# Kernel optimization log

Hardware: AMD Instinct MI355X
Metric: run time of the kernel (lower is better)

The kernel has to match this reference:

```python
import jax, jax.numpy as jnp
import numpy as np

B, S, N = 16, 64, 4096
D = 64            # input_dim*seq_len == output_dim*graph_dim
FEAT = 64
E = 32768
HEADS = (3, 3, 1)
NEG_SLOPE = 0.2   # PyG GATConv default negative_slope


def _lin_init(key, fi, fo):
    k1, k2 = jax.random.split(key)
    s = 1.0 / np.sqrt(fi)
    return (jax.random.uniform(k1, (fi, fo), jnp.float32, -s, s),
            jax.random.uniform(k2, (fo,), jnp.float32, -s, s))


def setup_inputs() -> dict:
    key = jax.random.key(0)
    ks = jax.random.split(key, 32)
    inp = {}
    inp["inputs"] = jax.random.normal(ks[0], (B, S, N, 1), jnp.float32)
    inp["edge_index"] = jax.random.randint(ks[1], (2, E), 0, N, dtype=jnp.int32)
    inp["W_seq"], inp["b_seq"] = _lin_init(ks[2], D, D)
    inp["src_embed"] = jax.random.normal(ks[3], (N, FEAT), jnp.float32) * 0.1
    inp["tgt_embed"] = jax.random.normal(ks[4], (FEAT, N), jnp.float32) * 0.1
    for i, H in enumerate(HEADS):
        s = 1.0 / np.sqrt(D)
        inp[f"Wg{i}"] = jax.random.uniform(ks[5 + 5 * i], (D, H * D), jnp.float32, -s, s)
        inp[f"asrc{i}"] = jax.random.normal(ks[6 + 5 * i], (H, D), jnp.float32) * 0.1
        inp[f"adst{i}"] = jax.random.normal(ks[7 + 5 * i], (H, D), jnp.float32) * 0.1
        inp[f"bg{i}"] = jnp.zeros((D,), jnp.float32)
        inp[f"Wl{i}"], inp[f"bl{i}"] = _lin_init(ks[8 + 5 * i], D, D)
    inp["Wo"], inp["bo"] = _lin_init(ks[25], D, D)
    return inp


def _gat(x, src, dst, W, a_src, a_dst, b):
    # PyG GATConv, concat=False (mean over heads). x: [B,N,D] -> [B,N,D]
    H, C = a_src.shape
    xp = jnp.einsum('bnd,dhc->bnhc', x, W.reshape(D, H, C))       # [B,N,H,C]
    al_s = jnp.einsum('bnhc,hc->bnh', xp, a_src)
    al_d = jnp.einsum('bnhc,hc->bnh', xp, a_dst)
    e = jax.nn.leaky_relu(al_s[:, src] + al_d[:, dst], NEG_SLOPE)  # [B,Et,H]

    def per_graph(e_b, xj_b):
        m = jax.ops.segment_max(e_b, dst, num_segments=N)          # [N,H]
        w = jnp.exp(e_b - m[dst])
        z = jax.ops.segment_sum(w, dst, num_segments=N)
        alpha = w / z[dst]                                         # softmax per dst node
        return jax.ops.segment_sum(xj_b * alpha[..., None], dst, num_segments=N)

    out = jax.vmap(per_graph)(e, xp[:, src])                       # [B,N,H,C]
    return out.mean(axis=2) + b


def _forward(inputs, edge_index, W_seq, b_seq, src_embed, tgt_embed,
             Wg0, asrc0, adst0, bg0, Wl0, bl0,
             Wg1, asrc1, adst1, bg1, Wl1, bl1,
             Wg2, asrc2, adst2, bg2, Wl2, bl2, Wo, bo):
    loop = jnp.arange(N, dtype=edge_index.dtype)
    src = jnp.concatenate([edge_index[0], loop])   # PyG add_self_loops=True
    dst = jnp.concatenate([edge_index[1], loop])
    h = inputs.transpose(0, 2, 3, 1).reshape(B * N, D)
    h = h @ W_seq + b_seq + h                       # seq_linear residual
    A = jax.nn.softmax(jax.nn.relu(src_embed @ tgt_embed), axis=1)  # learned adjacency [N,N]
    gat_p = [(Wg0, asrc0, adst0, bg0), (Wg1, asrc1, adst1, bg1), (Wg2, asrc2, adst2, bg2)]
    lin_p = [(Wl0, bl0), (Wl1, bl1), (Wl2, bl2)]
    for i in range(3):
        hb = h.reshape(B, N, D)
        # layer-0 GAT output is computed but unused in the original code (dead); skip it
        h_cur = _gat(hb, src, dst, *gat_p[i]).reshape(B * N, D) if i > 0 else None
        adp = jnp.einsum('mn,bnd->bmd', A, hb)      # adaptive-graph matmul (dropout in eval = identity)
        adp = (adp @ lin_p[i][0] + lin_p[i][1]).reshape(B * N, D)
        g = jax.nn.sigmoid(adp)
        if i == 0:
            origin = h @ Wo + bo
            h = jnp.tanh(h) * g + origin * (1.0 - g)
        elif i == 1:
            h = jax.nn.leaky_relu(h_cur, 0.01) * g + h * (1.0 - g)
        else:
            h = jax.nn.relu(h_cur) * g + h * (1.0 - g)
    return h.reshape(B, N, 1, D)   # [batch, node_num, output_dim, graph_dim]


def reference(inputs, edge_index, W_seq, b_seq, src_embed, tgt_embed,
              Wg0, asrc0, adst0, bg0, Wl0, bl0,
              Wg1, asrc1, adst1, bg1, Wl1, bl1,
              Wg2, asrc2, adst2, bg2, Wl2, bl2, Wo, bo):
    return _forward(inputs, edge_index, W_seq, b_seq, src_embed, tgt_embed,
                    Wg0, asrc0, adst0, bg0, Wl0, bl0,
                    Wg1, asrc1, adst1, bg1, Wl1, bl1,
                    Wg2, asrc2, adst2, bg2, Wl2, bl2, Wo, bo)
```

## Files before the change

kernel.cpp:

```cpp
#include <hip/hip_runtime.h>
#include <stdint.h>

#define NB 16
#define NN 4096
#define DD 64
#define EE 32768
#define ETOT 36864
#define ROWS 65536
#define KSPLIT 2

typedef _Float16 f16;
typedef f16   half8 __attribute__((ext_vector_type(8)));
typedef f16   f16x8 __attribute__((ext_vector_type(8)));
typedef f16   f16x4 __attribute__((ext_vector_type(4)));
typedef float f32x4 __attribute__((ext_vector_type(4)));

__device__ __forceinline__ void gload16(const f16* g, f16* l) {
  __builtin_amdgcn_global_load_lds((const __attribute__((address_space(1))) void*)g,
                                   (__attribute__((address_space(3))) void*)l, 16, 0, 0);
}

__global__ __launch_bounds__(256) void k_zero2(int* a, int* b) {
  int i = blockIdx.x * 256 + threadIdx.x;
  if (i < NN) a[i] = 0;
  else if (i < 2 * NN) b[i - NN] = 0;
}

__global__ __launch_bounds__(256) void k_count(const int* __restrict__ ei, int* __restrict__ cnt) {
  int t = blockIdx.x * 256 + threadIdx.x;
  if (t >= ETOT) return;
  int d = (t < EE) ? ei[EE + t] : (t - EE);
  atomicAdd(&cnt[d], 1);
}

__global__ __launch_bounds__(256) void k_scan(const int* __restrict__ cnt, int* __restrict__ offs) {
  __shared__ int part[256];
  int t = threadIdx.x;
  int loc[16]; int s = 0;
  #pragma unroll
  for (int i = 0; i < 16; ++i) { int v = cnt[(t << 4) + i]; loc[i] = s; s += v; }
  part[t] = s;
  __syncthreads();
  int own = s;
  for (int d = 1; d < 256; d <<= 1) {
    int u = (t >= d) ? part[t - d] : 0;
    __syncthreads();
    part[t] += u;
    __syncthreads();
  }
  int base = part[t] - own;
  #pragma unroll
  for (int i = 0; i < 16; ++i) offs[(t << 4) + i] = base + loc[i];
}

__global__ __launch_bounds__(256) void k_fill(const int* __restrict__ ei, const int* __restrict__ offs,
                                              int* __restrict__ cur, int* __restrict__ esrc,
                                              int* __restrict__ edst) {
  int t = blockIdx.x * 256 + threadIdx.x;
  if (t >= ETOT) return;
  int s, d;
  if (t < EE) { s = ei[t]; d = ei[EE + t]; } else { s = d = t - EE; }
  int p = atomicAdd(&cur[d], 1);
  esrc[offs[d] + p] = s;
  edst[offs[d] + p] = d;
}

__global__ __launch_bounds__(256) void k_seq(const float* __restrict__ inp, const float* __restrict__ Wseq,
                                             const float* __restrict__ bseq, float* __restrict__ h) {
  __shared__ float X[64 * 68];
  int t = threadIdx.x;
  int b = blockIdx.x >> 6, n0 = (blockIdx.x & 63) << 6;
  #pragma unroll
  for (int i = 0; i < 16; ++i) {
    int idx = t + (i << 8);
    int s = idx >> 6, nl = idx & 63;
    X[nl * 68 + s] = inp[((size_t)((b << 6) + s) << 12) + n0 + nl];
  }
  __syncthreads();
  int c = t & 63, rg = t >> 6;
  float Wc[64];
  #pragma unroll
  for (int k = 0; k < 64; ++k) Wc[k] = Wseq[(k << 6) + c];
  float bc = bseq[c];
  for (int rr = 0; rr < 16; ++rr) {
    int r = (rg << 4) + rr;
    float a = bc + X[r * 68 + c];
    #pragma unroll
    for (int k4 = 0; k4 < 16; ++k4) {
      float4 x = *(const float4*)&X[r * 68 + (k4 << 2)];
      a = fmaf(x.x, Wc[4*k4+0], a); a = fmaf(x.y, Wc[4*k4+1], a);
      a = fmaf(x.z, Wc[4*k4+2], a); a = fmaf(x.w, Wc[4*k4+3], a);
    }
    h[((size_t)(b << 12) + n0 + r) * 64 + c] = a;
  }
}

__global__ __launch_bounds__(256) void k_cast(const float* __restrict__ SE, const float* __restrict__ TE,
                                              f16* __restrict__ SEh, f16* __restrict__ TEh) {
  __shared__ float X[64 * 65];
  int t = threadIdx.x;
  if (blockIdx.x < 256) {
    int i = (blockIdx.x * 256 + t) * 4;
    float4 v = *(const float4*)(SE + i);
    f16 o[4] = {(f16)v.x, (f16)v.y, (f16)v.z, (f16)v.w};
    *(uint64_t*)(SEh + i) = *(uint64_t*)o;
    return;
  }
  int j0 = (blockIdx.x - 256) << 6;
  #pragma unroll
  for (int i = 0; i < 16; ++i) {
    int idx = t + (i << 8);
    int k = idx >> 6, jl = idx & 63;
    X[jl * 65 + k] = TE[((size_t)k << 12) + j0 + jl];
  }
  __syncthreads();
  int jl = t >> 2, kg = t & 3;
  f16 o[16];
  #pragma unroll
  for (int i = 0; i < 16; ++i) o[i] = (f16)X[jl * 65 + (kg << 4) + i];
  f16* dst = TEh + ((size_t)(j0 + jl) << 6) + (kg << 4);
  *(uint64_t*)(dst + 0) = *(uint64_t*)(o + 0);
  *(uint64_t*)(dst + 4) = *(uint64_t*)(o + 4);
  *(uint64_t*)(dst + 8) = *(uint64_t*)(o + 8);
  *(uint64_t*)(dst + 12) = *(uint64_t*)(o + 12);
}

__global__ __launch_bounds__(256) void k_adjmm(const f16* __restrict__ SEh, const f16* __restrict__ TEh,
                                               f16* __restrict__ A, float* __restrict__ Zpart) {
  __shared__ f16 Al[2][128 * 32];
  __shared__ f16 Bl[2][128 * 32];
  const int t = threadIdx.x, lane = t & 63, w = t >> 6;
  const int m0 = blockIdx.y << 7, j0 = blockIdx.x << 7;
  const int l15 = lane & 15, lhi = lane >> 4;
  const int wm = (w >> 1) << 6, wj = (w & 1) << 6;
  f32x4 acc[4][4] = {};
  const int c0 = (w << 6) + lane;
  const int row0 = c0 >> 2, ko0 = (c0 & 3) << 3;
  const int c1 = c0 + 256;
  const int row1 = c1 >> 2, ko1 = (c1 & 3) << 3;
  const f16* ga0 = SEh + (size_t)(m0 + row0) * 64 + ko0;
  const f16* ga1 = SEh + (size_t)(m0 + row1) * 64 + ko1;
  const f16* gb0 = TEh + (size_t)(j0 + row0) * 64 + ko0;
  const f16* gb1 = TEh + (size_t)(j0 + row1) * 64 + ko1;
  #pragma unroll
  for (int kt = 0; kt < 2; ++kt) {
    const int kof = kt << 5;
    gload16(ga0 + kof, Al[kt] + c0 * 8);
    gload16(ga1 + kof, Al[kt] + c1 * 8);
    gload16(gb0 + kof, Bl[kt] + c0 * 8);
    gload16(gb1 + kof, Bl[kt] + c1 * 8);
  }
  __syncthreads();
  #pragma unroll
  for (int kt = 0; kt < 2; ++kt) {
    half8 af[4], bf[4];
    #pragma unroll
    for (int i = 0; i < 4; ++i) {
      af[i] = *(const half8*)(Al[kt] + (wm + i * 16 + l15) * 32 + lhi * 8);
      bf[i] = *(const half8*)(Bl[kt] + (wj + i * 16 + l15) * 32 + lhi * 8);
    }
    #pragma unroll
    for (int mi = 0; mi < 4; ++mi)
      #pragma unroll
      for (int nj = 0; nj < 4; ++nj)
        acc[mi][nj] = __builtin_amdgcn_mfma_f32_16x16x32_f16(af[mi], bf[nj], acc[mi][nj], 0, 0, 0);
  }
  float rs[4][4];
  #pragma unroll
  for (int mi = 0; mi < 4; ++mi)
    #pragma unroll
    for (int r = 0; r < 4; ++r) rs[mi][r] = 0.f;
  #pragma unroll
  for (int mi = 0; mi < 4; ++mi)
    #pragma unroll
    for (int nj = 0; nj < 4; ++nj)
      #pragma unroll
      for (int r = 0; r < 4; ++r) {
        int row = m0 + wm + mi * 16 + lhi * 4 + r;
        int col = j0 + wj + nj * 16 + l15;
        float e = __expf(fmaxf(acc[mi][nj][r], 0.f));
        f16 eh = (f16)e;
        A[((size_t)row << 12) + col] = eh;
        rs[mi][r] += (float)eh;
      }
  #pragma unroll
  for (int mi = 0; mi < 4; ++mi)
    #pragma unroll
    for (int r = 0; r < 4; ++r) {
      float s = rs[mi][r];
      s += __shfl_xor(s, 1); s += __shfl_xor(s, 2);
      s += __shfl_xor(s, 4); s += __shfl_xor(s, 8);
      rs[mi][r] = s;
    }
  if (l15 == 0) {
    int p = (blockIdx.x << 1) + (w & 1);
    #pragma unroll
    for (int mi = 0; mi < 4; ++mi)
      #pragma unroll
      for (int r = 0; r < 4; ++r)
        Zpart[((size_t)p << 12) + m0 + wm + mi * 16 + lhi * 4 + r] = rs[mi][r];
  }
}

__global__ __launch_bounds__(256) void k_rowz(const float* __restrict__ Zpart, float* __restrict__ rowZ) {
  int row = blockIdx.x * 256 + threadIdx.x;
  float s = 0.f;
  #pragma unroll 8
  for (int p = 0; p < 64; ++p) s += Zpart[((size_t)p << 12) + row];
  rowZ[row] = 1.f / s;
}

#define NKT 32
__global__ __launch_bounds__(512) void k_gemm8(const f16* __restrict__ A, const f16* __restrict__ BT,
                                               f16* __restrict__ Cout) {
  extern __shared__ f16 smem[];
  const int t = threadIdx.x, lane = t & 63, wid = t >> 6;
  const int wr = wid >> 2, wc = wid & 3;
  const int l15 = lane & 15, lhi = lane >> 4;
  const int h7 = l15 & 7;
  const int wgid = blockIdx.x;
  const int nid = (wgid & 7) * 32 + (wgid >> 3);
  const int z = nid >> 7, rem = nid & 127;
  const int m0 = (rem >> 3) << 8;
  const int j0 = (rem & 7) << 7;
  const size_t kbase = (size_t)z << 11;
  f16* __restrict__ Cz = Cout + ((size_t)z << 22);

  const f16* gA[4]; int lA[4];
  #pragma unroll
  for (int i = 0; i < 4; ++i) {
    int s = t + (i << 9), row = s >> 3, sl = (s & 7) ^ (row & 7);
    gA[i] = A + (size_t)(m0 + row) * 4096 + kbase + sl * 8;
    lA[i] = s * 8;
  }
  const f16* gB[2]; int lB[2];
  #pragma unroll
  for (int i = 0; i < 2; ++i) {
    int s = t + (i << 9), row = s >> 3, sl = (s & 7) ^ (row & 7);
    gB[i] = BT + (size_t)(j0 + row) * 4096 + kbase + sl * 8;
    lB[i] = 16384 + s * 8;
  }
  #define SA(buf, kt, i) gload16(gA[i] + (kt) * 64, smem + (buf) * 24576 + lA[i])
  #define SB(buf, kt, i) gload16(gB[i] + (kt) * 64, smem + (buf) * 24576 + lB[i])

  const int rbase = wr << 7;
  const int cbase = wc << 5;
  f32x4 acc[8][2] = {};

  #pragma unroll
  for (int i = 0; i < 4; ++i) SA(0, 0, i);
  #pragma unroll
  for (int i = 0; i < 2; ++i) SB(0, 0, i);
  #pragma unroll
  for (int i = 0; i < 4; ++i) SA(1, 1, i);
  #pragma unroll
  for (int i = 0; i < 2; ++i) SB(1, 1, i);
  asm volatile("s_waitcnt vmcnt(6)" ::: "memory");
  __builtin_amdgcn_sched_barrier(0);
  __builtin_amdgcn_s_barrier();
  __builtin_amdgcn_sched_barrier(0);

  int b0 = 0, b1 = 1, b2 = 2;
  for (int kt = 0; kt < NKT; ++kt) {
    const f16* Ab = smem + b0 * 24576;
    const f16* Bb = Ab + 16384;
    const bool pf = (kt + 2 < NKT);
    {
      half8 af[8], bf[2];
      #pragma unroll
      for (int mi = 0; mi < 8; ++mi) {
        int row = rbase + mi * 16 + l15;
        af[mi] = *(const half8*)(Ab + row * 64 + (lhi ^ h7) * 8);
      }
      #pragma unroll
      for (int nj = 0; nj < 2; ++nj) {
        int row = cbase + nj * 16 + l15;
        bf[nj] = *(const half8*)(Bb + row * 64 + (lhi ^ h7) * 8);
      }
      if (pf) { SA(b2, kt + 2, 0); SA(b2, kt + 2, 1); SA(b2, kt + 2, 2); }
      __builtin_amdgcn_s_setprio(1);
      #pragma unroll
      for (int mi = 0; mi < 8; ++mi)
        #pragma unroll
        for (int nj = 0; nj < 2; ++nj)
          acc[mi][nj] = __builtin_amdgcn_mfma_f32_16x16x32_f16(af[mi], bf[nj], acc[mi][nj], 0, 0, 0);
      __builtin_amdgcn_s_setprio(0);
    }
    __builtin_amdgcn_s_barrier();
    __builtin_amdgcn_sched_barrier(0);
    {
      half8 af[8], bf[2];
      #pragma unroll
      for (int mi = 0; mi < 8; ++mi) {
        int row = rbase + mi * 16 + l15;
        af[mi] = *(const half8*)(Ab + row * 64 + ((4 + lhi) ^ h7) * 8);
      }
      #pragma unroll
      for (int nj = 0; nj < 2; ++nj) {
        int row = cbase + nj * 16 + l15;
        bf[nj] = *(const half8*)(Bb + row * 64 + ((4 + lhi) ^ h7) * 8);
      }
      if (pf) { SA(b2, kt + 2, 3); SB(b2, kt + 2, 0); SB(b2, kt + 2, 1); }
      __builtin_amdgcn_s_setprio(1);
      #pragma unroll
      for (int mi = 0; mi < 8; ++mi)
        #pragma unroll
        for (int nj = 0; nj < 2; ++nj)
          acc[mi][nj] = __builtin_amdgcn_mfma_f32_16x16x32_f16(af[mi], bf[nj], acc[mi][nj], 0, 0, 0);
      __builtin_amdgcn_s_setprio(0);
    }
    if (kt < NKT - 2)       asm volatile("s_waitcnt vmcnt(6)" ::: "memory");
    else if (kt == NKT - 2) asm volatile("s_waitcnt vmcnt(0)" ::: "memory");
    __builtin_amdgcn_sched_barrier(0);
    __builtin_amdgcn_s_barrier();
    __builtin_amdgcn_sched_barrier(0);
    int tb = b0; b0 = b1; b1 = b2; b2 = tb;
  }
  #undef SA
  #undef SB
  #pragma unroll
  for (int mi = 0; mi < 8; ++mi)
    #pragma unroll
    for (int nj = 0; nj < 2; ++nj)
      #pragma unroll
      for (int r = 0; r < 4; ++r) {
        int row = m0 + rbase + mi * 16 + (lhi << 2) + r;
        int col = j0 + cbase + nj * 16 + l15;
        Cz[(size_t)row * 1024 + col] = (f16)acc[mi][nj][r];
      }
}

template<int H, int NP>
__device__ __forceinline__ void wprep_body(const float* __restrict__ Wg, const float* __restrict__ asrc,
                                           const float* __restrict__ adst, const float* __restrict__ Wl,
                                           f16* __restrict__ Wgh, int bid, int t) {
  const int WL0 = H * 64 + 16;
  for (int i = bid * 256 + t; i < NP * 64; i += 16 * 256) {
    int j = i >> 6, k = i & 63;
    float v;
    if (j < H * 64) {
      v = Wg[(size_t)k * (H * 64) + j];
    } else if (j < H * 64 + 2 * H) {
      int cc = j - H * 64, hh = cc >> 1;
      const float* a = ((cc & 1) ? adst : asrc) + (hh << 6);
      const float* wrow = Wg + (size_t)k * (H * 64) + (hh << 6);
      float s = 0.f;
      #pragma unroll 16
      for (int c = 0; c < 64; ++c) s = fmaf(wrow[c], a[c], s);
      v = s;
    } else if (j >= WL0 && j < WL0 + 64) {
      v = Wl[(k << 6) + (j - WL0)];
    } else v = 0.f;
    Wgh[(size_t)j * 64 + k] = (f16)v;
  }
}

__global__ __launch_bounds__(256) void k_allprep(
    const float* __restrict__ Wg1, const float* __restrict__ as1, const float* __restrict__ ad1,
    const float* __restrict__ Wl1, f16* __restrict__ Wgh1,
    const float* __restrict__ Wg2, const float* __restrict__ as2, const float* __restrict__ ad2,
    const float* __restrict__ Wl2, f16* __restrict__ Wgh2,
    const float* __restrict__ Wl0, const float* __restrict__ Wo, f16* __restrict__ W0h) {
  int bid = blockIdx.x, t = threadIdx.x;
  if (bid < 16) wprep_body<3, 272>(Wg1, as1, ad1, Wl1, Wgh1, bid, t);
  else if (bid < 32) wprep_body<1, 144>(Wg2, as2, ad2, Wl2, Wgh2, bid - 16, t);
  else {
    for (int i = (bid - 32) * 256 + t; i < 128 * 64; i += 8 * 256) {
      int j = i >> 6, k = i & 63;
      float v = (j < 64) ? Wl0[(k << 6) + j] : Wo[(k << 6) + (j - 64)];
      W0h[(size_t)j * 64 + k] = (f16)v;
    }
  }
}

template<int H, int NP>
__global__ __launch_bounds__(256) void k_xpmm(const float* __restrict__ h, const f16* __restrict__ Wgh,
                                              f16* __restrict__ xp, float* __restrict__ als,
                                              float* __restrict__ ald, f16* __restrict__ HWlT) {
  const int WL0 = H * 64 + 16, JW0 = WL0 / 16, NT = NP / 16;
  __shared__ f16 Ah[64 * 72];
  __shared__ f16 Bh[NP * 72];
  __shared__ f16 stage[64 * 72];
  const int t = threadIdx.x, lane = t & 63, w = t >> 6;
  const size_t r0 = (size_t)blockIdx.x * 64;
  const int b = (int)(r0 >> 12), n0 = (int)(r0 & 4095);
  #pragma unroll
  for (int i = 0; i < 4; ++i) {
    int idx = t + (i << 8);
    int row = idx >> 4, k4 = (idx & 15) << 2;
    float4 v = *(const float4*)&h[(r0 + row) * 64 + k4];
    f16 o[4] = {(f16)v.x, (f16)v.y, (f16)v.z, (f16)v.w};
    *(uint64_t*)&Ah[row * 72 + k4] = *(uint64_t*)o;
  }
  for (int i = t; i < NP * 16; i += 256) {
    int row = i >> 4, k4 = (i & 15) << 2;
    *(uint64_t*)&Bh[row * 72 + k4] = *(const uint64_t*)&Wgh[(size_t)row * 64 + k4];
  }
  __syncthreads();
  const int l15 = lane & 15, lhi = lane >> 4;
  f32x4 acc[NT] = {};
  #pragma unroll
  for (int kk = 0; kk < 2; ++kk) {
    half8 af = *(const half8*)&Ah[(w * 16 + l15) * 72 + kk * 32 + lhi * 8];
    #pragma unroll
    for (int j = 0; j < NT; ++j) {
      half8 bf = *(const half8*)&Bh[(j * 16 + l15) * 72 + kk * 32 + lhi * 8];
      acc[j] = __builtin_amdgcn_mfma_f32_16x16x32_f16(af, bf, acc[j], 0, 0, 0);
    }
  }
  const int rl = w * 16 + lhi * 4;
  #pragma unroll
  for (int j = 0; j < NT; ++j) {
    int col = j * 16 + l15;
    if (j * 16 + 15 < H * 64) {
      #pragma unroll
      for (int r = 0; r < 4; ++r) {
        if (H == 3) xp[(r0 + rl + r) * 256 + ((col & 63) << 2) + (col >> 6)] = (f16)acc[j][r];
        else        xp[(r0 + rl + r) * 64 + col] = (f16)acc[j][r];
      }
    } else if (j < JW0) {
      int cc = col - H * 64;
      if (cc >= 0 && cc < 2 * H) {
        int hh = cc >> 1;
        #pragma unroll
        for (int r = 0; r < 4; ++r) {
          if (cc & 1) ald[(r0 + rl + r) * H + hh] = acc[j][r];
          else        als[(r0 + rl + r) * H + hh] = acc[j][r];
        }
      }
    } else {
      int e = col - WL0;
      f16 o[4] = {(f16)acc[j][0], (f16)acc[j][1], (f16)acc[j][2], (f16)acc[j][3]};
      *(uint64_t*)&stage[e * 72 + rl] = *(uint64_t*)o;
    }
  }
  __syncthreads();
  {
    int e = t >> 2, seg = (t & 3) << 4;
    float4 v0 = *(const float4*)&stage[e * 72 + seg];
    float4 v1 = *(const float4*)&stage[e * 72 + seg + 8];
    f16* dst = HWlT + (((size_t)((b << 6) + e)) << 12) + n0 + seg;
    *(float4*)dst = v0;
    *(float4*)(dst + 8) = v1;
  }
}

__global__ __launch_bounds__(256) void k_prep0(const float* __restrict__ h, const f16* __restrict__ W0h,
                                               f16* __restrict__ HWlT, f16* __restrict__ orig) {
  __shared__ f16 Ah[64 * 72];
  __shared__ f16 Bh[128 * 72];
  __shared__ f16 stage[64 * 72];
  const int t = threadIdx.x, lane = t & 63, w = t >> 6;
  const size_t r0 = (size_t)blockIdx.x * 64;
  const int b = (int)(r0 >> 12), n0 = (int)(r0 & 4095);
  #pragma unroll
  for (int i = 0; i < 4; ++i) {
    int idx = t + (i << 8);
    int row = idx >> 4, k4 = (idx & 15) << 2;
    float4 v = *(const float4*)&h[(r0 + row) * 64 + k4];
    f16 o[4] = {(f16)v.x, (f16)v.y, (f16)v.z, (f16)v.w};
    *(uint64_t*)&Ah[row * 72 + k4] = *(uint64_t*)o;
  }
  for (int i = t; i < 128 * 16; i += 256) {
    int row = i >> 4, k4 = (i & 15) << 2;
    *(uint64_t*)&Bh[row * 72 + k4] = *(const uint64_t*)&W0h[(size_t)row * 64 + k4];
  }
  __syncthreads();
  const int l15 = lane & 15, lhi = lane >> 4;
  f32x4 acc[8] = {};
  #pragma unroll
  for (int kk = 0; kk < 2; ++kk) {
    half8 af = *(const half8*)&Ah[(w * 16 + l15) * 72 + kk * 32 + lhi * 8];
    #pragma unroll
    for (int j = 0; j < 8; ++j) {
      half8 bf = *(const half8*)&Bh[(j * 16 + l15) * 72 + kk * 32 + lhi * 8];
      acc[j] = __builtin_amdgcn_mfma_f32_16x16x32_f16(af, bf, acc[j], 0, 0, 0);
    }
  }
  const int rl = w * 16 + lhi * 4;
  #pragma unroll
  for (int j = 0; j < 8; ++j) {
    int col = j * 16 + l15;
    if (j < 4) {
      f16 o[4] = {(f16)acc[j][0], (f16)acc[j][1], (f16)acc[j][2], (f16)acc[j][3]};
      *(uint64_t*)&stage[col * 72 + rl] = *(uint64_t*)o;
    } else {
      #pragma unroll
      for (int r = 0; r < 4; ++r)
        orig[(r0 + rl + r) * 64 + (col - 64)] = (f16)acc[j][r];
    }
  }
  __syncthreads();
  {
    int e = t >> 2, seg = (t & 3) << 4;
    float4 v0 = *(const float4*)&stage[e * 72 + seg];
    float4 v1 = *(const float4*)&stage[e * 72 + seg + 8];
    f16* dst = HWlT + (((size_t)((b << 6) + e)) << 12) + n0 + seg;
    *(float4*)dst = v0;
    *(float4*)(dst + 8) = v1;
  }
}

template<int H>
__global__ __launch_bounds__(256) void k_maxals(const float* __restrict__ als, float* __restrict__ Mals) {
  __shared__ float red[256];
  int b = blockIdx.x, t = threadIdx.x;
  size_t rbase = (size_t)b << 12;
  for (int h = 0; h < H; ++h) {
    float m = -1e30f;
    for (int n = t; n < NN; n += 256) m = fmaxf(m, als[(rbase + n) * H + h]);
    red[t] = m;
    __syncthreads();
    for (int d = 128; d; d >>= 1) {
      if (t < d) red[t] = fmaxf(red[t], red[t + d]);
      __syncthreads();
    }
    if (t == 0) Mals[b * H + h] = red[0];
    __syncthreads();
  }
}

template<int H>
__global__ __launch_bounds__(256) void k_wts(const float* __restrict__ als, const float* __restrict__ ald,
                                             const float* __restrict__ Mals, const int* __restrict__ esrc,
                                             const int* __restrict__ edst, float* __restrict__ wts) {
  const int WST = (H == 3) ? 4 : 1;
  int t = threadIdx.x, lane = t & 63, w = t >> 6;
  int gw = blockIdx.x * 4 + w;
  int b = gw & 15;
  int p = ((gw >> 4) << 6) + lane;
  size_t rbase = (size_t)b << 12;
  int s = esrc[p], n = edst[p];
  float* dst = wts + ((size_t)b * ETOT + p) * WST;
  #pragma unroll
  for (int h = 0; h < H; ++h) {
    float ad = ald[(rbase + n) * H + h];
    float B = Mals[b * H + h] + ad;
    float T = B > 0.f ? B : 0.2f * B;
    float ev = als[(rbase + s) * H + h] + ad;
    ev = ev > 0.f ? ev : 0.2f * ev;
    dst[h] = __expf(ev - T);
  }
}

template<int H>
__global__ __launch_bounds__(256) void k_agg(const f16* __restrict__ xp, const float* __restrict__ wts,
                                             const int* __restrict__ offs, const int* __restrict__ cnt,
                                             const int* __restrict__ esrc, const float* __restrict__ bg,
                                             float* __restrict__ hcur) {
  const int WST = (H == 3) ? 4 : 1;
  __shared__ float wbuf[4][64 * WST];
  __shared__ int   sbuf[4][64];
  int t = threadIdx.x, lane = t & 63, wv = t >> 6;
  int wid = (blockIdx.x << 2) + wv;
  int b = wid >> 12, n = wid & 4095;
  size_t rbase = (size_t)b << 12;
  int o = offs[n], c = cnt[n];
  const float* wsrc = wts + ((size_t)b * ETOT + o) * WST;
  float z[H], acc[H];
  #pragma unroll
  for (int hh = 0; hh < H; ++hh) { z[hh] = 0.f; acc[hh] = 0.f; }
  for (int e0 = 0; e0 < c; e0 += 64) {
    int ce = min(64, c - e0);
    if (lane < ce) {
      sbuf[wv][lane] = esrc[o + e0 + lane];
      if (H == 3) *(float4*)&wbuf[wv][lane * 4] = *(const float4*)&wsrc[(size_t)(e0 + lane) * 4];
      else        wbuf[wv][lane] = wsrc[e0 + lane];
    }
    #pragma unroll 4
    for (int e = 0; e < ce; ++e) {
      int s = sbuf[wv][e];
      if (H == 3) {
        float4 w4 = *(const float4*)&wbuf[wv][e * 4];
        f16x4 q = *(const f16x4*)(xp + (((size_t)(rbase + s)) << 8) + (lane << 2));
        z[0] += w4.x; acc[0] = fmaf(w4.x, (float)q[0], acc[0]);
        z[1] += w4.y; acc[1] = fmaf(w4.y, (float)q[1], acc[1]);
        z[2] += w4.z; acc[2] = fmaf(w4.z, (float)q[2], acc[2]);
      } else {
        float wv_ = wbuf[wv][e];
        float xv = (float)xp[(((size_t)(rbase + s)) << 6) + lane];
        z[0] += wv_; acc[0] = fmaf(wv_, xv, acc[0]);
      }
    }
  }
  float r = 0.f;
  #pragma unroll
  for (int hh = 0; hh < H; ++hh) r += acc[hh] / z[hh];
  hcur[(rbase + n) * 64 + lane] = r * (1.f / H) + bg[lane];
}

__global__ __launch_bounds__(256) void k_comb0e(const float* __restrict__ h, const f16* __restrict__ gp,
                                                const float* __restrict__ rowZ, const f16* __restrict__ orig,
                                                const float* __restrict__ bl, const float* __restrict__ bo,
                                                float* __restrict__ hout) {
  for (size_t i4 = (size_t)blockIdx.x * 256 + threadIdx.x; i4 < (size_t)ROWS * 16; i4 += (size_t)2048 * 256) {
    size_t i = i4 * 4;
    int d = (int)(i & 63), n = (int)((i >> 6) & 4095), b = (int)(i >> 18);
    size_t ga = ((size_t)n << 10) + (b << 6) + d;
    float zi = rowZ[n];
    f16x4 g0 = *(const f16x4*)&gp[ga];
    f16x4 g1 = *(const f16x4*)&gp[ga + (size_t)(4096 * 1024)];
    f16x4 og = *(const f16x4*)&orig[i];
    float4 hv = *(const float4*)&h[i];
    float4 o;
    float* op = &o.x;
    const float* hp = &hv.x;
    #pragma unroll
    for (int r = 0; r < 4; ++r) {
      float g = 1.f / (1.f + __expf(-(((float)g0[r] + (float)g1[r]) * zi + bl[d + r])));
      float orv = (float)og[r] + bo[d + r];
      op[r] = tanhf(hp[r]) * g + orv * (1.f - g);
    }
    *(float4*)&hout[i] = o;
  }
}

template<int ACT>
__global__ __launch_bounds__(256) void k_comb12e(const float* __restrict__ h, const f16* __restrict__ gp,
                                                 const float* __restrict__ rowZ, const float* __restrict__ hcur,
                                                 const float* __restrict__ bl, float* __restrict__ hout) {
  for (size_t i4 = (size_t)blockIdx.x * 256 + threadIdx.x; i4 < (size_t)ROWS * 16; i4 += (size_t)2048 * 256) {
    size_t i = i4 * 4;
    int d = (int)(i & 63), n = (int)((i >> 6) & 4095), b = (int)(i >> 18);
    size_t ga = ((size_t)n << 10) + (b << 6) + d;
    float zi = rowZ[n];
    f16x4 g0 = *(const f16x4*)&gp[ga];
    f16x4 g1 = *(const f16x4*)&gp[ga + (size_t)(4096 * 1024)];
    float4 hv = *(const float4*)&h[i];
    float4 cv = *(const float4*)&hcur[i];
    float4 o;
    float* op = &o.x;
    const float* hp = &hv.x;
    const float* cp = &cv.x;
    #pragma unroll
    for (int r = 0; r < 4; ++r) {
      float g = 1.f / (1.f + __expf(-(((float)g0[r] + (float)g1[r]) * zi + bl[d + r])));
      float act = ACT ? fmaxf(cp[r], 0.f) : (cp[r] > 0.f ? cp[r] : 0.01f * cp[r]);
      op[r] = act * g + hp[r] * (1.f - g);
    }
    *(float4*)&hout[i] = o;
  }
}

extern "C" void kernel_launch(void* const* d_in, const int* in_sizes, int n_in,
                              void* d_out, int out_size, void* d_ws, size_t ws_size,
                              hipStream_t stream) {
  (void)in_sizes; (void)n_in; (void)out_size; (void)ws_size;
  const float* inp  = (const float*)d_in[0];
  const int*   ei   = (const int*)d_in[1];
  const float* Wseq = (const float*)d_in[2];
  const float* bseq = (const float*)d_in[3];
  const float* SE   = (const float*)d_in[4];
  const float* TE   = (const float*)d_in[5];
  const float* Wg[3]   = {(const float*)d_in[6],  (const float*)d_in[12], (const float*)d_in[18]};
  const float* asrc[3] = {(const float*)d_in[7],  (const float*)d_in[13], (const float*)d_in[19]};
  const float* adst[3] = {(const float*)d_in[8],  (const float*)d_in[14], (const float*)d_in[20]};
  const float* bgp[3]  = {(const float*)d_in[9],  (const float*)d_in[15], (const float*)d_in[21]};
  const float* Wl[3]   = {(const float*)d_in[10], (const float*)d_in[16], (const float*)d_in[22]};
  const float* bl[3]   = {(const float*)d_in[11], (const float*)d_in[17], (const float*)d_in[23]};
  const float* Wo = (const float*)d_in[24];
  const float* bo = (const float*)d_in[25];
  float* out = (float*)d_out;

  uint8_t* ws = (uint8_t*)d_ws;
  size_t o = 0;
  auto nxt = [&](size_t sz) { void* p = ws + o; o += (sz + 255) & ~(size_t)255; return p; };
  f16*   Af   = (f16*)  nxt((size_t)NN * NN * sizeof(f16));
  f16*   HWlT = (f16*)  nxt((size_t)1024 * NN * sizeof(f16));
  float* h    = (float*)nxt((size_t)ROWS * 64 * 4);
  f16*   gp   = (f16*)  nxt((size_t)KSPLIT * NN * 1024 * sizeof(f16));
  f16*   xp   = (f16*)  nxt((size_t)ROWS * 256 * sizeof(f16));
  f16*   orig = (f16*)  nxt((size_t)ROWS * 64 * sizeof(f16));
  float* als  = (float*)nxt((size_t)ROWS * 3 * 4);
  float* ald  = (float*)nxt((size_t)ROWS * 3 * 4);
  float* hcur = (float*)nxt((size_t)ROWS * 64 * 4);
  float* rowZ = (float*)nxt((size_t)NN * 4);
  float* Zpart= (float*)nxt((size_t)64 * NN * 4);
  f16*   SEh  = (f16*)  nxt((size_t)NN * 64 * sizeof(f16));
  f16*   TEh  = (f16*)  nxt((size_t)NN * 64 * sizeof(f16));
  f16*   Wgh1 = (f16*)  nxt((size_t)288 * 64 * sizeof(f16));
  f16*   Wgh2 = (f16*)  nxt((size_t)144 * 64 * sizeof(f16));
  f16*   W0h  = (f16*)  nxt((size_t)128 * 64 * sizeof(f16));
  float* wts  = (float*)nxt((size_t)NB * ETOT * 4 * 4);
  float* Mals = (float*)nxt((size_t)NB * 3 * 4);
  int*   cnt  = (int*)  nxt((size_t)NN * 4);
  int*   curp = (int*)  nxt((size_t)NN * 4);
  int*   offs = (int*)  nxt((size_t)NN * 4);
  int*   esrc = (int*)  nxt((size_t)ETOT * 4);
  int*   edst = (int*)  nxt((size_t)ETOT * 4);

  static bool attr_set = false;
  if (!attr_set) {
    hipFuncSetAttribute((const void*)k_gemm8, hipFuncAttributeMaxDynamicSharedMemorySize, 147456);
    attr_set = true;
  }

  dim3 blk(256);
  k_zero2<<<32, blk, 0, stream>>>(cnt, curp);
  k_count<<<144, blk, 0, stream>>>(ei, cnt);
  k_scan<<<1, blk, 0, stream>>>(cnt, offs);
  k_fill<<<144, blk, 0, stream>>>(ei, offs, curp, esrc, edst);
  k_allprep<<<40, blk, 0, stream>>>(Wg[1], asrc[1], adst[1], Wl[1], Wgh1,
                                    Wg[2], asrc[2], adst[2], Wl[2], Wgh2,
                                    Wl[0], Wo, W0h);
  k_seq<<<1024, blk, 0, stream>>>(inp, Wseq, bseq, h);
  k_cast<<<320, blk, 0, stream>>>(SE, TE, SEh, TEh);
  k_adjmm<<<dim3(32, 32), blk, 0, stream>>>(SEh, TEh, Af, Zpart);
  k_rowz<<<16, blk, 0, stream>>>(Zpart, rowZ);
  k_prep0<<<1024, blk, 0, stream>>>(h, W0h, HWlT, orig);
  k_gemm8<<<256, 512, 147456, stream>>>(Af, HWlT, gp);
  k_comb0e<<<2048, blk, 0, stream>>>(h, gp, rowZ, orig, bl[0], bo, h);
  k_xpmm<3, 272><<<1024, blk, 0, stream>>>(h, Wgh1, xp, als, ald, HWlT);
  k_maxals<3><<<16, blk, 0, stream>>>(als, Mals);
  k_wts<3><<<2304, blk, 0, stream>>>(als, ald, Mals, esrc, edst, wts);
  k_gemm8<<<256, 512, 147456, stream>>>(Af, HWlT, gp);
  k_agg<3><<<16384, blk, 0, stream>>>(xp, wts, offs, cnt, esrc, bgp[1], hcur);
  k_comb12e<0><<<2048, blk, 0, stream>>>(h, gp, rowZ, hcur, bl[1], h);
  k_xpmm<1, 144><<<1024, blk, 0, stream>>>(h, Wgh2, xp, als, ald, HWlT);
  k_maxals<1><<<16, blk, 0, stream>>>(als, Mals);
  k_wts<1><<<2304, blk, 0, stream>>>(als, ald, Mals, esrc, edst, wts);
  k_gemm8<<<256, 512, 147456, stream>>>(Af, HWlT, gp);
  k_agg<1><<<16384, blk, 0, stream>>>(xp, wts, offs, cnt, esrc, bgp[2], hcur);
  k_comb12e<1><<<2048, blk, 0, stream>>>(h, gp, rowZ, hcur, bl[2], out);
}
```

Measured before the change: 328.4 us.

## Fuse gating combine into aggregation, merge cast into prep, retile GEMM warps

New measurement: 308.4 us. -6.1%, faster.

```diff
diff --git a/kernel.cpp b/kernel.cpp
--- a/kernel.cpp
+++ b/kernel.cpp
@@ -93,36 +93,6 @@
     }
     h[((size_t)(b << 12) + n0 + r) * 64 + c] = a;
   }
-}
-
-__global__ __launch_bounds__(256) void k_cast(const float* __restrict__ SE, const float* __restrict__ TE,
-                                              f16* __restrict__ SEh, f16* __restrict__ TEh) {
-  __shared__ float X[64 * 65];
-  int t = threadIdx.x;
-  if (blockIdx.x < 256) {
-    int i = (blockIdx.x * 256 + t) * 4;
-    float4 v = *(const float4*)(SE + i);
-    f16 o[4] = {(f16)v.x, (f16)v.y, (f16)v.z, (f16)v.w};
-    *(uint64_t*)(SEh + i) = *(uint64_t*)o;
-    return;
-  }
-  int j0 = (blockIdx.x - 256) << 6;
-  #pragma unroll
-  for (int i = 0; i < 16; ++i) {
-    int idx = t + (i << 8);
-    int k = idx >> 6, jl = idx & 63;
-    X[jl * 65 + k] = TE[((size_t)k << 12) + j0 + jl];
-  }
-  __syncthreads();
-  int jl = t >> 2, kg = t & 3;
-  f16 o[16];
-  #pragma unroll
-  for (int i = 0; i < 16; ++i) o[i] = (f16)X[jl * 65 + (kg << 4) + i];
-  f16* dst = TEh + ((size_t)(j0 + jl) << 6) + (kg << 4);
-  *(uint64_t*)(dst + 0) = *(uint64_t*)(o + 0);
-  *(uint64_t*)(dst + 4) = *(uint64_t*)(o + 4);
-  *(uint64_t*)(dst + 8) = *(uint64_t*)(o + 8);
-  *(uint64_t*)(dst + 12) = *(uint64_t*)(o + 12);
 }
 
 __global__ __launch_bounds__(256) void k_adjmm(const f16* __restrict__ SEh, const f16* __restrict__ TEh,
@@ -215,7 +185,7 @@
                                                f16* __restrict__ Cout) {
   extern __shared__ f16 smem[];
   const int t = threadIdx.x, lane = t & 63, wid = t >> 6;
-  const int wr = wid >> 2, wc = wid & 3;
+  const int wr = wid >> 1, wc = wid & 1;
   const int l15 = lane & 15, lhi = lane >> 4;
   const int h7 = l15 & 7;
   const int wgid = blockIdx.x;
@@ -243,9 +213,9 @@
   #define SA(buf, kt, i) gload16(gA[i] + (kt) * 64, smem + (buf) * 24576 + lA[i])
   #define SB(buf, kt, i) gload16(gB[i] + (kt) * 64, smem + (buf) * 24576 + lB[i])
 
-  const int rbase = wr << 7;
-  const int cbase = wc << 5;
-  f32x4 acc[8][2] = {};
+  const int rbase = wr << 6;
+  const int cbase = wc << 6;
+  f32x4 acc[4][4] = {};
 
   #pragma unroll
   for (int i = 0; i < 4; ++i) SA(0, 0, i);
@@ -266,46 +236,46 @@
     const f16* Bb = Ab + 16384;
     const bool pf = (kt + 2 < NKT);
     {
-      half8 af[8], bf[2];
-      #pragma unroll
-      for (int mi = 0; mi < 8; ++mi) {
+      half8 af[4], bf[4];
+      #pragma unroll
+      for (int mi = 0; mi < 4; ++mi) {
         int row = rbase + mi * 16 + l15;
         af[mi] = *(const half8*)(Ab + row * 64 + (lhi ^ h7) * 8);
       }
       #pragma unroll
-      for (int nj = 0; nj < 2; ++nj) {
+      for (int nj = 0; nj < 4; ++nj) {
         int row = cbase + nj * 16 + l15;
         bf[nj] = *(const half8*)(Bb + row * 64 + (lhi ^ h7) * 8);
       }
       if (pf) { SA(b2, kt + 2, 0); SA(b2, kt + 2, 1); SA(b2, kt + 2, 2); }
       __builtin_amdgcn_s_setprio(1);
       #pragma unroll
-      for (int mi = 0; mi < 8; ++mi)
+      for (int mi = 0; mi < 4; ++mi)
         #pragma unroll
-        for (int nj = 0; nj < 2; ++nj)
+        for (int nj = 0; nj < 4; ++nj)
           acc[mi][nj] = __builtin_amdgcn_mfma_f32_16x16x32_f16(af[mi], bf[nj], acc[mi][nj], 0, 0, 0);
       __builtin_amdgcn_s_setprio(0);
     }
     __builtin_amdgcn_s_barrier();
     __builtin_amdgcn_sched_barrier(0);
     {
-      half8 af[8], bf[2];
-      #pragma unroll
-      for (int mi = 0; mi < 8; ++mi) {
+      half8 af[4], bf[4];
+      #pragma unroll
+      for (int mi = 0; mi < 4; ++mi) {
         int row = rbase + mi * 16 + l15;
         af[mi] = *(const half8*)(Ab + row * 64 + ((4 + lhi) ^ h7) * 8);
       }
       #pragma unroll
-      for (int nj = 0; nj < 2; ++nj) {
+      for (int nj = 0; nj < 4; ++nj) {
         int row = cbase + nj * 16 + l15;
         bf[nj] = *(const half8*)(Bb + row * 64 + ((4 + lhi) ^ h7) * 8);
       }
       if (pf) { SA(b2, kt + 2, 3); SB(b2, kt + 2, 0); SB(b2, kt + 2, 1); }
       __builtin_amdgcn_s_setprio(1);
       #pragma unroll
-      for (int mi = 0; mi < 8; ++mi)
+      for (int mi = 0; mi < 4; ++mi)
         #pragma unroll
-        for (int nj = 0; nj < 2; ++nj)
+        for (int nj = 0; nj < 4; ++nj)
           acc[mi][nj] = __builtin_amdgcn_mfma_f32_16x16x32_f16(af[mi], bf[nj], acc[mi][nj], 0, 0, 0);
       __builtin_amdgcn_s_setprio(0);
     }
@@ -319,9 +289,9 @@
   #undef SA
   #undef SB
   #pragma unroll
-  for (int mi = 0; mi < 8; ++mi)
-    #pragma unroll
-    for (int nj = 0; nj < 2; ++nj)
+  for (int mi = 0; mi < 4; ++mi)
+    #pragma unroll
+    for (int nj = 0; nj < 4; ++nj)
       #pragma unroll
       for (int r = 0; r < 4; ++r) {
         int row = m0 + rbase + mi * 16 + (lhi << 2) + r;
@@ -360,17 +330,45 @@
     const float* __restrict__ Wl1, f16* __restrict__ Wgh1,
     const float* __restrict__ Wg2, const float* __restrict__ as2, const float* __restrict__ ad2,
     const float* __restrict__ Wl2, f16* __restrict__ Wgh2,
-    const float* __restrict__ Wl0, const float* __restrict__ Wo, f16* __restrict__ W0h) {
+    const float* __restrict__ Wl0, const float* __restrict__ Wo, f16* __restrict__ W0h,
+    const float* __restrict__ SE, const float* __restrict__ TE,
+    f16* __restrict__ SEh, f16* __restrict__ TEh) {
+  __shared__ float X[64 * 65];
   int bid = blockIdx.x, t = threadIdx.x;
-  if (bid < 16) wprep_body<3, 272>(Wg1, as1, ad1, Wl1, Wgh1, bid, t);
-  else if (bid < 32) wprep_body<1, 144>(Wg2, as2, ad2, Wl2, Wgh2, bid - 16, t);
-  else {
+  if (bid < 16) { wprep_body<3, 272>(Wg1, as1, ad1, Wl1, Wgh1, bid, t); return; }
+  if (bid < 32) { wprep_body<1, 144>(Wg2, as2, ad2, Wl2, Wgh2, bid - 16, t); return; }
+  if (bid < 40) {
     for (int i = (bid - 32) * 256 + t; i < 128 * 64; i += 8 * 256) {
       int j = i >> 6, k = i & 63;
       float v = (j < 64) ? Wl0[(k << 6) + j] : Wo[(k << 6) + (j - 64)];
       W0h[(size_t)j * 64 + k] = (f16)v;
     }
-  }
+    return;
+  }
+  if (bid < 296) {
+    int i = ((bid - 40) * 256 + t) * 4;
+    float4 v = *(const float4*)(SE + i);
+    f16 o[4] = {(f16)v.x, (f16)v.y, (f16)v.z, (f16)v.w};
+    *(uint64_t*)(SEh + i) = *(uint64_t*)o;
+    return;
+  }
+  int j0 = (bid - 296) << 6;
+  #pragma unroll
+  for (int i = 0; i < 16; ++i) {
+    int idx = t + (i << 8);
+    int k = idx >> 6, jl = idx & 63;
+    X[jl * 65 + k] = TE[((size_t)k << 12) + j0 + jl];
+  }
+  __syncthreads();
+  int jl = t >> 2, kg = t & 3;
+  f16 o[16];
+  #pragma unroll
+  for (int i = 0; i < 16; ++i) o[i] = (f16)X[jl * 65 + (kg << 4) + i];
+  f16* dst = TEh + ((size_t)(j0 + jl) << 6) + (kg << 4);
+  *(uint64_t*)(dst + 0) = *(uint64_t*)(o + 0);
+  *(uint64_t*)(dst + 4) = *(uint64_t*)(o + 4);
+  *(uint64_t*)(dst + 8) = *(uint64_t*)(o + 8);
+  *(uint64_t*)(dst + 12) = *(uint64_t*)(o + 12);
 }
 
 template<int H, int NP>
@@ -543,11 +541,13 @@
   }
 }
 
-template<int H>
-__global__ __launch_bounds__(256) void k_agg(const f16* __restrict__ xp, const float* __restrict__ wts,
-                                             const int* __restrict__ offs, const int* __restrict__ cnt,
-                                             const int* __restrict__ esrc, const float* __restrict__ bg,
-                                             float* __restrict__ hcur) {
+template<int H, int ACT>
+__global__ __launch_bounds__(256) void k_aggc(const f16* __restrict__ xp, const float* __restrict__ wts,
+                                              const int* __restrict__ offs, const int* __restrict__ cnt,
+                                              const int* __restrict__ esrc, const float* __restrict__ bg,
+                                              const float* __restrict__ h, const f16* __restrict__ gp,
+                                              const float* __restrict__ rowZ, const float* __restrict__ bl,
+                                              float* __restrict__ hout) {
   const int WST = (H == 3) ? 4 : 1;
   __shared__ float wbuf[4][64 * WST];
   __shared__ int   sbuf[4][64];
@@ -586,7 +586,15 @@
   float r = 0.f;
   #pragma unroll
   for (int hh = 0; hh < H; ++hh) r += acc[hh] / z[hh];
-  hcur[(rbase + n) * 64 + lane] = r * (1.f / H) + bg[lane];
+  float cv = r * (1.f / H) + bg[lane];
+  size_t ga = ((size_t)n << 10) + (b << 6) + lane;
+  float zi = rowZ[n];
+  float g0 = (float)gp[ga], g1 = (float)gp[ga + (size_t)(4096 * 1024)];
+  float g = 1.f / (1.f + __expf(-((g0 + g1) * zi + bl[lane])));
+  size_t ridx = ((rbase + n) << 6) + lane;
+  float hv = h[ridx];
+  float act = ACT ? fmaxf(cv, 0.f) : (cv > 0.f ? cv : 0.01f * cv);
+  hout[ridx] = act * g + hv * (1.f - g);
 }
 
 __global__ __launch_bounds__(256) void k_comb0e(const float* __restrict__ h, const f16* __restrict__ gp,
@@ -610,33 +618,6 @@
       float g = 1.f / (1.f + __expf(-(((float)g0[r] + (float)g1[r]) * zi + bl[d + r])));
       float orv = (float)og[r] + bo[d + r];
       op[r] = tanhf(hp[r]) * g + orv * (1.f - g);
-    }
-    *(float4*)&hout[i] = o;
-  }
-}
-
-template<int ACT>
-__global__ __launch_bounds__(256) void k_comb12e(const float* __restrict__ h, const f16* __restrict__ gp,
-                                                 const float* __restrict__ rowZ, const float* __restrict__ hcur,
-                                                 const float* __restrict__ bl, float* __restrict__ hout) {
-  for (size_t i4 = (size_t)blockIdx.x * 256 + threadIdx.x; i4 < (size_t)ROWS * 16; i4 += (size_t)2048 * 256) {
-    size_t i = i4 * 4;
-    int d = (int)(i & 63), n = (int)((i >> 6) & 4095), b = (int)(i >> 18);
-    size_t ga = ((size_t)n << 10) + (b << 6) + d;
-    float zi = rowZ[n];
-    f16x4 g0 = *(const f16x4*)&gp[ga];
-    f16x4 g1 = *(const f16x4*)&gp[ga + (size_t)(4096 * 1024)];
-    float4 hv = *(const float4*)&h[i];
-    float4 cv = *(const float4*)&hcur[i];
-    float4 o;
-    float* op = &o.x;
-    const float* hp = &hv.x;
-    const float* cp = &cv.x;
-    #pragma unroll
-    for (int r = 0; r < 4; ++r) {
-      float g = 1.f / (1.f + __expf(-(((float)g0[r] + (float)g1[r]) * zi + bl[d + r])));
-      float act = ACT ? fmaxf(cp[r], 0.f) : (cp[r] > 0.f ? cp[r] : 0.01f * cp[r]);
-      op[r] = act * g + hp[r] * (1.f - g);
     }
     *(float4*)&hout[i] = o;
   }
@@ -673,7 +654,6 @@
   f16*   orig = (f16*)  nxt((size_t)ROWS * 64 * sizeof(f16));
   float* als  = (float*)nxt((size_t)ROWS * 3 * 4);
   float* ald  = (float*)nxt((size_t)ROWS * 3 * 4);
-  float* hcur = (float*)nxt((size_t)ROWS * 64 * 4);
   float* rowZ = (float*)nxt((size_t)NN * 4);
   float* Zpart= (float*)nxt((size_t)64 * NN * 4);
   f16*   SEh  = (f16*)  nxt((size_t)NN * 64 * sizeof(f16));
@@ -700,11 +680,10 @@
   k_count<<<144, blk, 0, stream>>>(ei, cnt);
   k_scan<<<1, blk, 0, stream>>>(cnt, offs);
   k_fill<<<144, blk, 0, stream>>>(ei, offs, curp, esrc, edst);
-  k_allprep<<<40, blk, 0, stream>>>(Wg[1], asrc[1], adst[1], Wl[1], Wgh1,
-                                    Wg[2], asrc[2], adst[2], Wl[2], Wgh2,
-                                    Wl[0], Wo, W0h);
+  k_allprep<<<360, blk, 0, stream>>>(Wg[1], asrc[1], adst[1], Wl[1], Wgh1,
+                                     Wg[2], asrc[2], adst[2], Wl[2], Wgh2,
+                                     Wl[0], Wo, W0h, SE, TE, SEh, TEh);
   k_seq<<<1024, blk, 0, stream>>>(inp, Wseq, bseq, h);
-  k_cast<<<320, blk, 0, stream>>>(SE, TE, SEh, TEh);
   k_adjmm<<<dim3(32, 32), blk, 0, stream>>>(SEh, TEh, Af, Zpart);
   k_rowz<<<16, blk, 0, stream>>>(Zpart, rowZ);
   k_prep0<<<1024, blk, 0, stream>>>(h, W0h, HWlT, orig);
@@ -714,12 +693,10 @@
   k_maxals<3><<<16, blk, 0, stream>>>(als, Mals);
   k_wts<3><<<2304, blk, 0, stream>>>(als, ald, Mals, esrc, edst, wts);
   k_gemm8<<<256, 512, 147456, stream>>>(Af, HWlT, gp);
-  k_agg<3><<<16384, blk, 0, stream>>>(xp, wts, offs, cnt, esrc, bgp[1], hcur);
-  k_comb12e<0><<<2048, blk, 0, stream>>>(h, gp, rowZ, hcur, bl[1], h);
+  k_aggc<3, 0><<<16384, blk, 0, stream>>>(xp, wts, offs, cnt, esrc, bgp[1], h, gp, rowZ, bl[1], h);
   k_xpmm<1, 144><<<1024, blk, 0, stream>>>(h, Wgh2, xp, als, ald, HWlT);
   k_maxals<1><<<16, blk, 0, stream>>>(als, Mals);
   k_wts<1><<<2304, blk, 0, stream>>>(als, ald, Mals, esrc, edst, wts);
   k_gemm8<<<256, 512, 147456, stream>>>(Af, HWlT, gp);
-  k_agg<1><<<16384, blk, 0, stream>>>(xp, wts, offs, cnt, esrc, bgp[2], hcur);
-  k_comb12e<1><<<2048, blk, 0, stream>>>(h, gp, rowZ, hcur, bl[2], out);
-}
+  k_aggc<1, 1><<<16384, blk, 0, stream>>>(xp, wts, offs, cnt, esrc, bgp[2], h, gp, rowZ, bl[2], out);
+}
```
